# Kernel optimization log

Measured on AMD Instinct MI355X. Metric: run time of the kernel, lower is better.

Reference implementation:

```python
import jax, jax.numpy as jnp
import numpy as np

# Config constants (from CantorExpertConfig)
EXPERT_ID = 2
NUM_EXPERTS = 8
FULL = 4096
EDIM = 1024
SLICE = FULL // NUM_EXPERTS            # 512
OVERLAP = 0.5
_base = 1.0 / NUM_EXPERTS
_ext = _base * OVERLAP
FP_MIN = max(0.0, EXPERT_ID / NUM_EXPERTS - _ext)          # 0.1875
FP_MAX = min(1.0, (EXPERT_ID + 1) / NUM_EXPERTS + _ext)    # 0.4375
SL_START = EXPERT_ID * SLICE
SL_END = SL_START + SLICE
B, P = 4, 4096


def setup_inputs() -> dict:
    key = jax.random.key(0)
    ks = jax.random.split(key, 10)
    tokens = jax.random.normal(ks[0], (B, P, FULL), jnp.float32)
    fingerprints = jax.random.uniform(ks[1], (P,), jnp.float32)
    # gate MLP: Linear(SLICE, SLICE//4) -> GELU -> Linear(SLICE//4, 1) -> Sigmoid
    W_g1 = jax.random.normal(ks[2], (SLICE // 4, SLICE), jnp.float32) / np.sqrt(SLICE)
    b_g1 = jnp.zeros((SLICE // 4,), jnp.float32)
    W_g2 = jax.random.normal(ks[3], (1, SLICE // 4), jnp.float32) / np.sqrt(SLICE // 4)
    b_g2 = jnp.zeros((1,), jnp.float32)
    alpha = jnp.float32(1.0)  # alpha_init
    # xavier-ish init, gain 0.5
    scale = 0.5 * np.sqrt(2.0 / (SLICE + EDIM))
    Wq = jax.random.normal(ks[4], (EDIM, SLICE), jnp.float32) * scale
    Wk = jax.random.normal(ks[5], (EDIM, SLICE), jnp.float32) * scale
    Wv = jax.random.normal(ks[6], (EDIM, SLICE), jnp.float32) * scale
    penta = jax.random.normal(ks[7], (5, EDIM), jnp.float32) * 0.02
    penta = penta / jnp.linalg.norm(penta, axis=-1, keepdims=True)
    return {
        "tokens": tokens, "fingerprints": fingerprints,
        "W_g1": W_g1, "b_g1": b_g1, "W_g2": W_g2, "b_g2": b_g2,
        "alpha": alpha, "Wq": Wq, "Wk": Wk, "Wv": Wv,
        "pentachoron": penta,
    }


def reference(tokens, fingerprints, W_g1, b_g1, W_g2, b_g2, alpha, Wq, Wk, Wv, pentachoron):
    # boolean fingerprint-region mask -> concrete gather indices (eager, outside jit)
    mask = (fingerprints >= FP_MIN) & (fingerprints < FP_MAX)
    idx = jnp.nonzero(mask)[0]                      # [Psel]
    # masked token gather + feature slice: [B, Psel, SLICE]
    my = tokens[:, idx, SL_START:SL_END]
    # gated-MLP alpha gate (torch GELU is exact/erf)
    h = jax.nn.gelu(my @ W_g1.T + b_g1, approximate=False)
    gate = jax.nn.sigmoid(h @ W_g2.T + b_g2)        # [B, Psel, 1]
    aw = jax.nn.sigmoid(alpha)
    my = my * (gate * aw + (1.0 - aw))
    # QKV projections (no bias)
    Q = my @ Wq.T                                   # [B, Psel, EDIM]
    K = my @ Wk.T
    V = my @ Wv.T
    # pentachoron 5-way vertex projections, batched over the 5 vertices
    dirs = pentachoron / jnp.linalg.norm(pentachoron, axis=-1, keepdims=True)  # [5, EDIM]
    Qp = jnp.einsum('bpd,vd->vbp', Q, dirs)         # [5, B, Psel]
    Kp = jnp.einsum('bpd,vd->vbp', K, dirs)
    Vp = jnp.einsum('bpd,vd->vbp', V, dirs)
    return (Q, K, V, Qp, Kp, Vp)
```

## Files before the change

kernel.cpp:

```cpp
#include <hip/hip_runtime.h>
#include <hip/hip_bf16.h>
#include <math.h>

#define PTOK 4096
#define BDIM 4
#define FULLD 4096
#define SLICE 512
#define SL_START 1024
#define EDIM 1024
#define FP_MIN_C 0.1875f
#define FP_MAX_C 0.4375f

typedef __attribute__((ext_vector_type(8))) short bf16x8;
typedef __attribute__((ext_vector_type(4))) float f32x4;

__device__ __forceinline__ unsigned short f2bf(float f) {
    unsigned int u = __float_as_uint(f);
    unsigned int r = (u + 0x7fffu + ((u >> 16) & 1u)) >> 16;
    return (unsigned short)r;
}

__device__ __forceinline__ void gl2lds16(const void* g, void* l) {
    __builtin_amdgcn_global_load_lds(
        (const __attribute__((address_space(1))) unsigned int*)g,
        (__attribute__((address_space(3))) unsigned int*)(unsigned long long)(uintptr_t)l,
        16, 0, 0);
}

__global__ __launch_bounds__(1024) void prep_kernel(const float* __restrict__ fp,
                                                    int* __restrict__ idx,
                                                    const float* __restrict__ penta,
                                                    float* __restrict__ dirs,
                                                    const float* __restrict__ Wq,
                                                    const float* __restrict__ Wk,
                                                    const float* __restrict__ Wv,
                                                    unsigned short* __restrict__ Wb) {
    int blk = blockIdx.x;
    int t = threadIdx.x;
    if (blk == 0) {
        int m[4];
        int c = 0;
#pragma unroll
        for (int i = 0; i < 4; ++i) {
            float f = fp[t * 4 + i];
            m[i] = (f >= FP_MIN_C && f < FP_MAX_C) ? 1 : 0;
            c += m[i];
        }
        int lane = t & 63, wv = t >> 6;
        int inc = c;
#pragma unroll
        for (int off = 1; off < 64; off <<= 1) {
            int n = __shfl_up(inc, off, 64);
            if (lane >= off) inc += n;
        }
        __shared__ int wsum[16];
        if (lane == 63) wsum[wv] = inc;
        __syncthreads();
        if (t < 16) {
            int v = wsum[t];
            int in2 = v;
#pragma unroll
            for (int off = 1; off < 16; off <<= 1) {
                int n = __shfl_up(in2, off, 16);
                if (t >= off) in2 += n;
            }
            wsum[t] = in2 - v;
        }
        __syncthreads();
        int pos = wsum[wv] + inc - c;
#pragma unroll
        for (int i = 0; i < 4; ++i) {
            if (m[i]) idx[pos++] = t * 4 + i;
        }
    } else if (blk <= 5) {
        int v = blk - 1;
        float4 p = make_float4(0.f, 0.f, 0.f, 0.f);
        float ss = 0.f;
        if (t < 256) {
            p = ((const float4*)(penta + (size_t)v * EDIM))[t];
            ss = p.x * p.x + p.y * p.y + p.z * p.z + p.w * p.w;
        }
        for (int off = 32; off > 0; off >>= 1) ss += __shfl_down(ss, off, 64);
        __shared__ float dsum[16];
        if ((t & 63) == 0) dsum[t >> 6] = ss;
        __syncthreads();
        if (t < 256) {
            float tot = dsum[0] + dsum[1] + dsum[2] + dsum[3];
            float inv = 1.0f / sqrtf(tot);
            float4 o = make_float4(p.x * inv, p.y * inv, p.z * inv, p.w * inv);
            ((float4*)(dirs + (size_t)v * EDIM))[t] = o;
        }
    } else {
        int i = (blk - 6) * 1024 + t;
        int mat = i >> 17;
        int rem = i & 131071;
        const float* src = (mat == 0) ? Wq : ((mat == 1) ? Wk : Wv);
        float4 v = ((const float4*)src)[rem];
        ushort4 o;
        o.x = f2bf(v.x); o.y = f2bf(v.y); o.z = f2bf(v.z); o.w = f2bf(v.w);
        ((ushort4*)(Wb + (size_t)mat * EDIM * SLICE))[rem] = o;
    }
}

#define GT 8
__global__ __launch_bounds__(256) void gate_kernel(const float* __restrict__ tokens,
                                                   const int* __restrict__ idx,
                                                   const float* __restrict__ Wg1,
                                                   const float* __restrict__ bg1,
                                                   const float* __restrict__ Wg2,
                                                   const float* __restrict__ bg2,
                                                   const float* __restrict__ alpha,
                                                   unsigned short* __restrict__ Ag,
                                                   int Ntok, int M) {
    __shared__ float rows[GT][SLICE];
    __shared__ float hred[GT][128];
    __shared__ float ssc[GT];

    int tid = threadIdx.x;
    int tok0 = blockIdx.x * GT;

#pragma unroll
    for (int i = 0; i < 4; ++i) {
        int flat = i * 256 + tid;
        int tk = flat >> 7, c4 = flat & 127;
        int g = tok0 + tk;
        if (g >= M) g = M - 1;
        int b = g / Ntok;
        int j = g - b * Ntok;
        int p = idx[j];
        const float4* src = (const float4*)(tokens + ((size_t)b * PTOK + p) * FULLD + SL_START);
        ((float4*)rows[tk])[c4] = src[c4];
    }
    __syncthreads();

    int hidx = tid & 127;
    int grp = tid >> 7;
    const float4* w4 = (const float4*)(Wg1 + (size_t)hidx * SLICE);
    float bias = bg1[hidx];
    float acc[4] = {bias, bias, bias, bias};
#pragma unroll 4
    for (int k = 0; k < SLICE / 4; ++k) {
        float4 w = w4[k];
#pragma unroll
        for (int t8 = 0; t8 < 4; ++t8) {
            float4 r = ((const float4*)rows[grp * 4 + t8])[k];
            acc[t8] += r.x * w.x + r.y * w.y + r.z * w.z + r.w * w.w;
        }
    }
    float wg2 = Wg2[hidx];
#pragma unroll
    for (int t8 = 0; t8 < 4; ++t8) {
        float a = acc[t8];
        float hg = 0.5f * a * (1.0f + erff(a * 0.70710678118654752f));
        hred[grp * 4 + t8][hidx] = hg * wg2;
    }
    __syncthreads();

    int wv = tid >> 6, l = tid & 63;
    float aw = 1.0f / (1.0f + expf(-alpha[0]));
#pragma unroll
    for (int z = 0; z < 2; ++z) {
        int tk = wv * 2 + z;
        float v = hred[tk][l] + hred[tk][l + 64];
        for (int off = 32; off > 0; off >>= 1) v += __shfl_down(v, off, 64);
        if (l == 0) {
            float logit = v + bg2[0];
            float gate = 1.0f / (1.0f + expf(-logit));
            ssc[tk] = gate * aw + (1.0f - aw);
        }
    }
    __syncthreads();

#pragma unroll
    for (int i = 0; i < 4; ++i) {
        int flat = i * 256 + tid;
        int tk = flat >> 7, c4 = flat & 127;
        int g = tok0 + tk;
        if (g < M) {
            float4 r = ((const float4*)rows[tk])[c4];
            float s = ssc[tk];
            ushort4 o;
            o.x = f2bf(r.x * s); o.y = f2bf(r.y * s);
            o.z = f2bf(r.z * s); o.w = f2bf(r.w * s);
            ((ushort4*)(Ag + (size_t)g * SLICE))[c4] = o;
        }
    }
}

__global__ __launch_bounds__(256) void qkv_mfma(const unsigned short* __restrict__ Ag,
                                                const unsigned short* __restrict__ Wb,
                                                float* __restrict__ out, int M) {
    __shared__ short As[2][128 * 32];
    __shared__ short Bs[2][128 * 32];

    const unsigned short* W = Wb + (size_t)blockIdx.z * EDIM * SLICE;
    float* C = out + (size_t)blockIdx.z * M * EDIM;

    int tid = threadIdx.x;
    int bm = blockIdx.y * 128;
    int bn = blockIdx.x * 128;
    int l = tid & 63;
    int w = tid >> 6;
    int wr = w >> 1, wc = w & 1;
    int lane16 = l & 15, kq = l >> 4;

    int srow = tid >> 2;
    int scol = (tid & 3) * 8;

    f32x4 acc[4][4] = {};

    for (int k0 = 0; k0 < SLICE; k0 += 64) {
#pragma unroll
        for (int p = 0; p < 2; ++p) {
#pragma unroll
            for (int r = 0; r < 2; ++r) {
                int arow = bm + r * 64 + srow;
                if (arow >= M) arow = M - 1;
                gl2lds16(Ag + (size_t)arow * SLICE + k0 + p * 32 + scol,
                         &As[p][(r * 64 + srow) * 32 + scol]);
                int brow = bn + r * 64 + srow;
                gl2lds16(W + (size_t)brow * SLICE + k0 + p * 32 + scol,
                         &Bs[p][(r * 64 + srow) * 32 + scol]);
            }
        }
        __syncthreads();

#pragma unroll
        for (int p = 0; p < 2; ++p) {
            bf16x8 a[4], b[4];
#pragma unroll
            for (int i = 0; i < 4; ++i)
                a[i] = *(const bf16x8*)&As[p][(wr * 64 + i * 16 + lane16) * 32 + kq * 8];
#pragma unroll
            for (int j = 0; j < 4; ++j)
                b[j] = *(const bf16x8*)&Bs[p][(wc * 64 + j * 16 + lane16) * 32 + kq * 8];
#pragma unroll
            for (int i = 0; i < 4; ++i)
#pragma unroll
                for (int j = 0; j < 4; ++j)
                    acc[i][j] = __builtin_amdgcn_mfma_f32_16x16x32_bf16(a[i], b[j], acc[i][j], 0, 0, 0);
        }
        __syncthreads();
    }

#pragma unroll
    for (int i = 0; i < 4; ++i) {
        int m0 = bm + wr * 64 + i * 16 + kq * 4;
#pragma unroll
        for (int j = 0; j < 4; ++j) {
            int n = bn + wc * 64 + j * 16 + lane16;
            f32x4 v = acc[i][j];
#pragma unroll
            for (int r = 0; r < 4; ++r) {
                int m = m0 + r;
                if (m < M) C[(size_t)m * EDIM + n] = v[r];
            }
        }
    }
}

__global__ __launch_bounds__(256) void proj_kernel(const float* __restrict__ qkv,
                                                   const float* __restrict__ dirs,
                                                   float* __restrict__ outp, int M) {
    __shared__ float dsh[5 * EDIM];
    int t = threadIdx.x;
#pragma unroll
    for (int i = 0; i < 5; ++i) {
        ((float4*)dsh)[i * 256 + t] = ((const float4*)dirs)[i * 256 + t];
    }
    __syncthreads();

    int gw = blockIdx.x * 4 + (t >> 6);
    if (gw >= 3 * M) return;
    int l = t & 63;
    int q = gw / M;
    int m = gw - q * M;

    const float4* row = (const float4*)(qkv + ((size_t)q * M + m) * EDIM);
    float acc[5] = {0.f, 0.f, 0.f, 0.f, 0.f};
#pragma unroll
    for (int it = 0; it < 4; ++it) {
        int c4 = it * 64 + l;
        float4 v = row[c4];
#pragma unroll
        for (int v5 = 0; v5 < 5; ++v5) {
            float4 d = ((const float4*)dsh)[v5 * 256 + c4];
            acc[v5] += v.x * d.x + v.y * d.y + v.z * d.z + v.w * d.w;
        }
    }
#pragma unroll
    for (int v5 = 0; v5 < 5; ++v5) {
        float a = acc[v5];
        for (int off = 32; off > 0; off >>= 1) a += __shfl_down(a, off, 64);
        if (l == 0) outp[(size_t)(q * 5 + v5) * M + m] = a;
    }
}

extern "C" void kernel_launch(void* const* d_in, const int* in_sizes, int n_in,
                              void* d_out, int out_size, void* d_ws, size_t ws_size,
                              hipStream_t stream) {
    const float* tokens = (const float*)d_in[0];
    const float* fp     = (const float*)d_in[1];
    const float* Wg1    = (const float*)d_in[2];
    const float* bg1    = (const float*)d_in[3];
    const float* Wg2    = (const float*)d_in[4];
    const float* bg2    = (const float*)d_in[5];
    const float* alpha  = (const float*)d_in[6];
    const float* Wq     = (const float*)d_in[7];
    const float* Wk     = (const float*)d_in[8];
    const float* Wv     = (const float*)d_in[9];
    const float* penta  = (const float*)d_in[10];
    float* out = (float*)d_out;

    int Ntok = out_size / 12348;
    int M = BDIM * Ntok;

    char* ws = (char*)d_ws;
    int*            idx  = (int*)ws;
    unsigned short* Ag   = (unsigned short*)(ws + (32 << 10));
    unsigned short* Wb   = (unsigned short*)(ws + (8 << 20));
    float*          dirs = (float*)(ws + (12 << 20));

    prep_kernel<<<390, 1024, 0, stream>>>(fp, idx, penta, dirs, Wq, Wk, Wv, Wb);
    gate_kernel<<<(M + GT - 1) / GT, 256, 0, stream>>>(tokens, idx, Wg1, bg1, Wg2, bg2,
                                                       alpha, Ag, Ntok, M);

    dim3 gg(EDIM / 128, (M + 127) / 128, 3);
    qkv_mfma<<<gg, 256, 0, stream>>>(Ag, Wb, out, M);

    proj_kernel<<<(3 * M + 3) / 4, 256, 0, stream>>>(out, dirs, out + (size_t)3 * M * EDIM, M);
}
```

Baseline: 387.8 us.

## Fuse pentachoron projections into QKV GEMM epilogue with atomic accumulation

After: 404.4 us. +4.3%, slower.

```diff
diff --git a/kernel.cpp b/kernel.cpp
--- a/kernel.cpp
+++ b/kernel.cpp
@@ -34,7 +34,9 @@
                                                     const float* __restrict__ Wq,
                                                     const float* __restrict__ Wk,
                                                     const float* __restrict__ Wv,
-                                                    unsigned short* __restrict__ Wb) {
+                                                    unsigned short* __restrict__ Wb,
+                                                    float* __restrict__ outz,
+                                                    int z4n) {
     int blk = blockIdx.x;
     int t = threadIdx.x;
     if (blk == 0) {
@@ -90,7 +92,7 @@
             float4 o = make_float4(p.x * inv, p.y * inv, p.z * inv, p.w * inv);
             ((float4*)(dirs + (size_t)v * EDIM))[t] = o;
         }
-    } else {
+    } else if (blk < 390) {
         int i = (blk - 6) * 1024 + t;
         int mat = i >> 17;
         int rem = i & 131071;
@@ -99,6 +101,9 @@
         ushort4 o;
         o.x = f2bf(v.x); o.y = f2bf(v.y); o.z = f2bf(v.z); o.w = f2bf(v.w);
         ((ushort4*)(Wb + (size_t)mat * EDIM * SLICE))[rem] = o;
+    } else {
+        int i = (blk - 390) * 1024 + t;
+        if (i < z4n) ((float4*)outz)[i] = make_float4(0.f, 0.f, 0.f, 0.f);
     }
 }
 
@@ -189,7 +194,9 @@
 
 __global__ __launch_bounds__(256) void qkv_mfma(const unsigned short* __restrict__ Ag,
                                                 const unsigned short* __restrict__ Wb,
-                                                float* __restrict__ out, int M) {
+                                                float* __restrict__ out, int M,
+                                                const float* __restrict__ dirs,
+                                                float* __restrict__ outp) {
     __shared__ short As[2][128 * 32];
     __shared__ short Bs[2][128 * 32];
 
@@ -257,42 +264,32 @@
             }
         }
     }
-}
-
-__global__ __launch_bounds__(256) void proj_kernel(const float* __restrict__ qkv,
-                                                   const float* __restrict__ dirs,
-                                                   float* __restrict__ outp, int M) {
-    __shared__ float dsh[5 * EDIM];
-    int t = threadIdx.x;
-#pragma unroll
-    for (int i = 0; i < 5; ++i) {
-        ((float4*)dsh)[i * 256 + t] = ((const float4*)dirs)[i * 256 + t];
-    }
-    __syncthreads();
-
-    int gw = blockIdx.x * 4 + (t >> 6);
-    if (gw >= 3 * M) return;
-    int l = t & 63;
-    int q = gw / M;
-    int m = gw - q * M;
-
-    const float4* row = (const float4*)(qkv + ((size_t)q * M + m) * EDIM);
-    float acc[5] = {0.f, 0.f, 0.f, 0.f, 0.f};
-#pragma unroll
-    for (int it = 0; it < 4; ++it) {
-        int c4 = it * 64 + l;
-        float4 v = row[c4];
-#pragma unroll
-        for (int v5 = 0; v5 < 5; ++v5) {
-            float4 d = ((const float4*)dsh)[v5 * 256 + c4];
-            acc[v5] += v.x * d.x + v.y * d.y + v.z * d.z + v.w * d.w;
-        }
-    }
+
+    float dv[5][4];
+#pragma unroll
+    for (int v5 = 0; v5 < 5; ++v5)
+#pragma unroll
+        for (int j = 0; j < 4; ++j)
+            dv[v5][j] = dirs[(size_t)v5 * EDIM + bn + wc * 64 + j * 16 + lane16];
+
+    float* op = outp + (size_t)(blockIdx.z * 5) * M;
 #pragma unroll
     for (int v5 = 0; v5 < 5; ++v5) {
-        float a = acc[v5];
-        for (int off = 32; off > 0; off >>= 1) a += __shfl_down(a, off, 64);
-        if (l == 0) outp[(size_t)(q * 5 + v5) * M + m] = a;
+#pragma unroll
+        for (int i = 0; i < 4; ++i) {
+#pragma unroll
+            for (int r = 0; r < 4; ++r) {
+                float s = acc[i][0][r] * dv[v5][0] + acc[i][1][r] * dv[v5][1]
+                        + acc[i][2][r] * dv[v5][2] + acc[i][3][r] * dv[v5][3];
+                s += __shfl_xor(s, 1, 64);
+                s += __shfl_xor(s, 2, 64);
+                s += __shfl_xor(s, 4, 64);
+                s += __shfl_xor(s, 8, 64);
+                int m = bm + wr * 64 + i * 16 + kq * 4 + r;
+                if (lane16 == 0 && m < M)
+                    atomicAdd(&op[(size_t)v5 * M + m], s);
+            }
+        }
     }
 }
 
@@ -321,12 +318,15 @@
     unsigned short* Wb   = (unsigned short*)(ws + (8 << 20));
     float*          dirs = (float*)(ws + (12 << 20));
 
-    prep_kernel<<<390, 1024, 0, stream>>>(fp, idx, penta, dirs, Wq, Wk, Wv, Wb);
+    float* outp = out + (size_t)3 * M * EDIM;
+    int z4 = (15 * M) / 4;
+    int zb = (z4 + 1023) / 1024;
+
+    prep_kernel<<<390 + zb, 1024, 0, stream>>>(fp, idx, penta, dirs, Wq, Wk, Wv, Wb,
+                                               outp, z4);
     gate_kernel<<<(M + GT - 1) / GT, 256, 0, stream>>>(tokens, idx, Wg1, bg1, Wg2, bg2,
                                                        alpha, Ag, Ntok, M);
 
     dim3 gg(EDIM / 128, (M + 127) / 128, 3);
-    qkv_mfma<<<gg, 256, 0, stream>>>(Ag, Wb, out, M);
-
-    proj_kernel<<<(3 * M + 3) / 4, 256, 0, stream>>>(out, dirs, out + (size_t)3 * M * EDIM, M);
-}
+    qkv_mfma<<<gg, 256, 0, stream>>>(Ag, Wb, out, M, dirs, outp);
+}
```

## Fold pentachoron directions into weights and project from gated activations

Applied to the files above, without the earlier changes.

Measured after the change: 408.4 us. +5.3%, slower.

```diff
diff --git a/kernel.cpp b/kernel.cpp
--- a/kernel.cpp
+++ b/kernel.cpp
@@ -30,11 +30,11 @@
 __global__ __launch_bounds__(1024) void prep_kernel(const float* __restrict__ fp,
                                                     int* __restrict__ idx,
                                                     const float* __restrict__ penta,
-                                                    float* __restrict__ dirs,
                                                     const float* __restrict__ Wq,
                                                     const float* __restrict__ Wk,
                                                     const float* __restrict__ Wv,
-                                                    unsigned short* __restrict__ Wb) {
+                                                    unsigned short* __restrict__ Wb,
+                                                    float* __restrict__ wproj) {
     int blk = blockIdx.x;
     int t = threadIdx.x;
     if (blk == 0) {
@@ -72,26 +72,8 @@
         for (int i = 0; i < 4; ++i) {
             if (m[i]) idx[pos++] = t * 4 + i;
         }
-    } else if (blk <= 5) {
-        int v = blk - 1;
-        float4 p = make_float4(0.f, 0.f, 0.f, 0.f);
-        float ss = 0.f;
-        if (t < 256) {
-            p = ((const float4*)(penta + (size_t)v * EDIM))[t];
-            ss = p.x * p.x + p.y * p.y + p.z * p.z + p.w * p.w;
-        }
-        for (int off = 32; off > 0; off >>= 1) ss += __shfl_down(ss, off, 64);
-        __shared__ float dsum[16];
-        if ((t & 63) == 0) dsum[t >> 6] = ss;
-        __syncthreads();
-        if (t < 256) {
-            float tot = dsum[0] + dsum[1] + dsum[2] + dsum[3];
-            float inv = 1.0f / sqrtf(tot);
-            float4 o = make_float4(p.x * inv, p.y * inv, p.z * inv, p.w * inv);
-            ((float4*)(dirs + (size_t)v * EDIM))[t] = o;
-        }
-    } else {
-        int i = (blk - 6) * 1024 + t;
+    } else if (blk <= 384) {
+        int i = (blk - 1) * 1024 + t;
         int mat = i >> 17;
         int rem = i & 131071;
         const float* src = (mat == 0) ? Wq : ((mat == 1) ? Wk : Wv);
@@ -99,6 +81,50 @@
         ushort4 o;
         o.x = f2bf(v.x); o.y = f2bf(v.y); o.z = f2bf(v.z); o.w = f2bf(v.w);
         ((ushort4*)(Wb + (size_t)mat * EDIM * SLICE))[rem] = o;
+    } else {
+        int zz = (blk - 385) >> 1;
+        int kh = (blk - 385) & 1;
+        __shared__ float dl[5 * EDIM + 8];
+        for (int i = t; i < 5 * EDIM; i += 1024) dl[i] = penta[i];
+        __syncthreads();
+        if (t < 320) {
+            int v = t >> 6, l = t & 63;
+            float ss = 0.f;
+            for (int i = l; i < EDIM; i += 64) {
+                float x = dl[v * EDIM + i];
+                ss += x * x;
+            }
+            for (int off = 32; off > 0; off >>= 1) ss += __shfl_down(ss, off, 64);
+            if (l == 0) dl[5 * EDIM + v] = 1.0f / sqrtf(ss);
+        }
+        __syncthreads();
+        int kk = t & 255;
+        int dq = t >> 8;
+        int k = kh * 256 + kk;
+        const float* Wz = (zz == 0) ? Wq : ((zz == 1) ? Wk : Wv);
+        float inv[5];
+#pragma unroll
+        for (int v = 0; v < 5; ++v) inv[v] = dl[5 * EDIM + v];
+        float acc[5] = {0.f, 0.f, 0.f, 0.f, 0.f};
+#pragma unroll 4
+        for (int d0 = 0; d0 < 256; ++d0) {
+            int d = dq * 256 + d0;
+            float w = Wz[(size_t)d * SLICE + k];
+#pragma unroll
+            for (int v = 0; v < 5; ++v) acc[v] += w * dl[v * EDIM + d];
+        }
+        __syncthreads();
+#pragma unroll
+        for (int v = 0; v < 5; ++v) dl[(dq * 5 + v) * 256 + kk] = acc[v] * inv[v];
+        __syncthreads();
+        if (t < 256) {
+#pragma unroll
+            for (int v = 0; v < 5; ++v) {
+                float s = dl[(0 + v) * 256 + t] + dl[(5 + v) * 256 + t]
+                        + dl[(10 + v) * 256 + t] + dl[(15 + v) * 256 + t];
+                wproj[((size_t)zz * 5 + v) * SLICE + kh * 256 + t] = s;
+            }
+        }
     }
 }
 
@@ -259,40 +285,30 @@
     }
 }
 
-__global__ __launch_bounds__(256) void proj_kernel(const float* __restrict__ qkv,
-                                                   const float* __restrict__ dirs,
-                                                   float* __restrict__ outp, int M) {
-    __shared__ float dsh[5 * EDIM];
+__global__ __launch_bounds__(256) void proj2_kernel(const unsigned short* __restrict__ Ag,
+                                                    const float* __restrict__ wproj,
+                                                    float* __restrict__ outp, int M) {
     int t = threadIdx.x;
-#pragma unroll
-    for (int i = 0; i < 5; ++i) {
-        ((float4*)dsh)[i * 256 + t] = ((const float4*)dirs)[i * 256 + t];
-    }
-    __syncthreads();
-
-    int gw = blockIdx.x * 4 + (t >> 6);
-    if (gw >= 3 * M) return;
+    int m = blockIdx.x * 4 + (t >> 6);
+    if (m >= M) return;
     int l = t & 63;
-    int q = gw / M;
-    int m = gw - q * M;
-
-    const float4* row = (const float4*)(qkv + ((size_t)q * M + m) * EDIM);
-    float acc[5] = {0.f, 0.f, 0.f, 0.f, 0.f};
-#pragma unroll
-    for (int it = 0; it < 4; ++it) {
-        int c4 = it * 64 + l;
-        float4 v = row[c4];
-#pragma unroll
-        for (int v5 = 0; v5 < 5; ++v5) {
-            float4 d = ((const float4*)dsh)[v5 * 256 + c4];
-            acc[v5] += v.x * d.x + v.y * d.y + v.z * d.z + v.w * d.w;
-        }
-    }
-#pragma unroll
-    for (int v5 = 0; v5 < 5; ++v5) {
-        float a = acc[v5];
-        for (int off = 32; off > 0; off >>= 1) a += __shfl_down(a, off, 64);
-        if (l == 0) outp[(size_t)(q * 5 + v5) * M + m] = a;
+
+    bf16x8 av = *(const bf16x8*)(Ag + (size_t)m * SLICE + (size_t)l * 8);
+    float a[8];
+#pragma unroll
+    for (int i = 0; i < 8; ++i)
+        a[i] = __uint_as_float(((unsigned int)(unsigned short)av[i]) << 16);
+
+#pragma unroll
+    for (int v = 0; v < 15; ++v) {
+        const float4* wp4 = (const float4*)(wproj + (size_t)v * SLICE);
+        float4 w0 = wp4[l * 2];
+        float4 w1 = wp4[l * 2 + 1];
+        float s = a[0] * w0.x + a[1] * w0.y + a[2] * w0.z + a[3] * w0.w
+                + a[4] * w1.x + a[5] * w1.y + a[6] * w1.z + a[7] * w1.w;
+#pragma unroll
+        for (int off = 32; off > 0; off >>= 1) s += __shfl_down(s, off, 64);
+        if (l == 0) outp[(size_t)v * M + m] = s;
     }
 }
 
@@ -316,17 +332,19 @@
     int M = BDIM * Ntok;
 
     char* ws = (char*)d_ws;
-    int*            idx  = (int*)ws;
-    unsigned short* Ag   = (unsigned short*)(ws + (32 << 10));
-    unsigned short* Wb   = (unsigned short*)(ws + (8 << 20));
-    float*          dirs = (float*)(ws + (12 << 20));
-
-    prep_kernel<<<390, 1024, 0, stream>>>(fp, idx, penta, dirs, Wq, Wk, Wv, Wb);
+    int*            idx   = (int*)ws;
+    unsigned short* Ag    = (unsigned short*)(ws + (32 << 10));
+    unsigned short* Wb    = (unsigned short*)(ws + (8 << 20));
+    float*          wproj = (float*)(ws + (12 << 20));
+
+    float* outp = out + (size_t)3 * M * EDIM;
+
+    prep_kernel<<<391, 1024, 0, stream>>>(fp, idx, penta, Wq, Wk, Wv, Wb, wproj);
     gate_kernel<<<(M + GT - 1) / GT, 256, 0, stream>>>(tokens, idx, Wg1, bg1, Wg2, bg2,
                                                        alpha, Ag, Ntok, M);
 
     dim3 gg(EDIM / 128, (M + 127) / 128, 3);
     qkv_mfma<<<gg, 256, 0, stream>>>(Ag, Wb, out, M);
 
-    proj_kernel<<<(3 * M + 3) / 4, 256, 0, stream>>>(out, dirs, out + (size_t)3 * M * EDIM, M);
-}
+    proj2_kernel<<<(M + 3) / 4, 256, 0, stream>>>(Ag, wproj, outp, M);
+}
```
